# Kernel optimization log

Hardware: AMD Instinct MI355X
Metric: run time of the kernel (lower is better)

## Reference

```python
import jax, jax.numpy as jnp
import numpy as np

EPS = 1e-12  # matches torch.nn.functional.normalize default eps

B, SQ, SD, H, D = 64, 128, 1024, 768, 128


def setup_inputs() -> dict:
    key = jax.random.key(0)
    k1, k2, k3 = jax.random.split(key, 3)
    return {
        "query_hidden": jax.random.normal(k1, (B, SQ, H), dtype=jnp.float32),
        "query_attention_mask": jnp.ones((B, SQ), dtype=jnp.int32),
        "doc_hidden": jax.random.normal(k2, (B, SD, H), dtype=jnp.float32),
        "doc_attention_mask": jnp.ones((B, SD), dtype=jnp.int32),
        "W": jax.random.normal(k3, (D, H), dtype=jnp.float32) * (H ** -0.5),
    }


def _encode(hidden, mask, W):
    # mask padding tokens, project hidden_size -> colbert_dim, L2 normalize per token
    emb = hidden * mask[..., None].astype(hidden.dtype)          # [b, s, h]
    emb = jnp.einsum("bsh,dh->bsd", emb, W)                      # [b, s, d]
    norm = jnp.linalg.norm(emb, axis=-1, keepdims=True)
    return emb / jnp.maximum(norm, EPS)


def reference(query_hidden, query_attention_mask, doc_hidden, doc_attention_mask, W):
    q = _encode(query_hidden, query_attention_mask, W)           # [b, sq, d]
    dcc = _encode(doc_hidden, doc_attention_mask, W)             # [b, sd, d]
    sim = jnp.einsum("bsd,btd->bst", q, dcc)                     # [b, sq, sd]
    return sim.max(axis=2).sum(axis=1)                           # [b] MaxSim score
```

## Files before the change

kernel.cpp:

```cpp
#include <hip/hip_runtime.h>
#include <hip/hip_bf16.h>

#define NB 64
#define SQL 128
#define SDL 1024
#define HH 768
#define DD 128

typedef __attribute__((ext_vector_type(8))) short short8;
typedef __attribute__((ext_vector_type(4))) float f32x4;

__device__ __forceinline__ unsigned short bf16r(float f) {
    unsigned int u = __builtin_bit_cast(unsigned int, f);
    u += 0x7FFFu + ((u >> 16) & 1u);
    return (unsigned short)(u >> 16);
}

__global__ __launch_bounds__(256) void k_wconv(const float* __restrict__ W,
                                               unsigned short* __restrict__ Wb) {
    int i = blockIdx.x * 256 + threadIdx.x;
    float4 v = reinterpret_cast<const float4*>(W)[i];
    ushort4 o;
    o.x = bf16r(v.x); o.y = bf16r(v.y); o.z = bf16r(v.z); o.w = bf16r(v.w);
    reinterpret_cast<ushort4*>(Wb)[i] = o;
}

__global__ __launch_bounds__(256) void k_project(
        const float* __restrict__ qh, const int* __restrict__ qm,
        const float* __restrict__ dh, const int* __restrict__ dm,
        const unsigned short* __restrict__ Wb,
        unsigned short* __restrict__ qe, unsigned short* __restrict__ de) {
    int bx = blockIdx.x;
    int b = bx / 9;
    int seg = bx % 9;
    const float* src;
    const int* mask;
    unsigned short* dst;
    if (seg == 0) {
        src = qh + (size_t)b * SQL * HH;
        mask = qm + (size_t)b * SQL;
        dst = qe + (size_t)b * SQL * DD;
    } else {
        size_t off = (size_t)(seg - 1) * 128;
        src = dh + ((size_t)b * SDL + off) * HH;
        mask = dm + (size_t)b * SDL + off;
        dst = de + ((size_t)b * SDL + off) * DD;
    }

    int lane = threadIdx.x & 63;
    int w = threadIdx.x >> 6;
    int l15 = lane & 15;
    int lg = lane >> 4;

    f32x4 acc[8][2];
#pragma unroll
    for (int dt = 0; dt < 8; ++dt)
#pragma unroll
        for (int jt = 0; jt < 2; ++jt) acc[dt][jt] = (f32x4){0.f, 0.f, 0.f, 0.f};

    const float* rowp0 = src + (size_t)(w * 32 + l15) * HH;
    const float* rowp1 = src + (size_t)(w * 32 + 16 + l15) * HH;

    for (int ks = 0; ks < HH / 32; ++ks) {
        int k0 = ks * 32 + lg * 8;
        short8 hf[2];
        {
            float4 a0 = *reinterpret_cast<const float4*>(rowp0 + k0);
            float4 a1 = *reinterpret_cast<const float4*>(rowp0 + k0 + 4);
            short8 s;
            s[0] = (short)bf16r(a0.x); s[1] = (short)bf16r(a0.y);
            s[2] = (short)bf16r(a0.z); s[3] = (short)bf16r(a0.w);
            s[4] = (short)bf16r(a1.x); s[5] = (short)bf16r(a1.y);
            s[6] = (short)bf16r(a1.z); s[7] = (short)bf16r(a1.w);
            hf[0] = s;
        }
        {
            float4 a0 = *reinterpret_cast<const float4*>(rowp1 + k0);
            float4 a1 = *reinterpret_cast<const float4*>(rowp1 + k0 + 4);
            short8 s;
            s[0] = (short)bf16r(a0.x); s[1] = (short)bf16r(a0.y);
            s[2] = (short)bf16r(a0.z); s[3] = (short)bf16r(a0.w);
            s[4] = (short)bf16r(a1.x); s[5] = (short)bf16r(a1.y);
            s[6] = (short)bf16r(a1.z); s[7] = (short)bf16r(a1.w);
            hf[1] = s;
        }
#pragma unroll
        for (int dt = 0; dt < 8; ++dt) {
            short8 wf = *reinterpret_cast<const short8*>(Wb + (size_t)(dt * 16 + l15) * HH + k0);
            acc[dt][0] = __builtin_amdgcn_mfma_f32_16x16x32_bf16(wf, hf[0], acc[dt][0], 0, 0, 0);
            acc[dt][1] = __builtin_amdgcn_mfma_f32_16x16x32_bf16(wf, hf[1], acc[dt][1], 0, 0, 0);
        }
    }

#pragma unroll
    for (int jt = 0; jt < 2; ++jt) {
        float ss = 0.f;
#pragma unroll
        for (int dt = 0; dt < 8; ++dt) {
            ss += acc[dt][jt][0] * acc[dt][jt][0];
            ss += acc[dt][jt][1] * acc[dt][jt][1];
            ss += acc[dt][jt][2] * acc[dt][jt][2];
            ss += acc[dt][jt][3] * acc[dt][jt][3];
        }
        ss += __shfl_xor(ss, 16, 64);
        ss += __shfl_xor(ss, 32, 64);
        int tokl = w * 32 + jt * 16 + l15;
        int mk = mask[tokl];
        float scale = mk ? (1.0f / fmaxf(sqrtf(ss), 1e-12f)) : 0.0f;
        unsigned short* orow = dst + (size_t)tokl * DD + lg * 4;
#pragma unroll
        for (int dt = 0; dt < 8; ++dt) {
            ushort4 o;
            o.x = bf16r(acc[dt][jt][0] * scale);
            o.y = bf16r(acc[dt][jt][1] * scale);
            o.z = bf16r(acc[dt][jt][2] * scale);
            o.w = bf16r(acc[dt][jt][3] * scale);
            *reinterpret_cast<ushort4*>(orow + dt * 16) = o;
        }
    }
}

__global__ __launch_bounds__(256) void k_sim(const unsigned short* __restrict__ qe,
                                             const unsigned short* __restrict__ de,
                                             float* __restrict__ partial) {
    __shared__ uint4 qs[SQL * 16];
    __shared__ uint4 dsm[256 * 16];
    __shared__ float bm[4][SQL];

    int b = blockIdx.x >> 2;
    int c = blockIdx.x & 3;

    const uint4* qg = reinterpret_cast<const uint4*>(qe + (size_t)b * SQL * DD);
    for (int idx = threadIdx.x; idx < SQL * 16; idx += 256) {
        int row = idx >> 4, ch = idx & 15;
        qs[row * 16 + (ch ^ (row & 7))] = qg[idx];
    }
    const uint4* dg = reinterpret_cast<const uint4*>(de + ((size_t)b * SDL + (size_t)c * 256) * DD);
    for (int idx = threadIdx.x; idx < 256 * 16; idx += 256) {
        int row = idx >> 4, ch = idx & 15;
        dsm[row * 16 + (ch ^ (row & 7))] = dg[idx];
    }
    __syncthreads();

    int lane = threadIdx.x & 63;
    int w = threadIdx.x >> 6;
    int l15 = lane & 15;
    int lg = lane >> 4;

    float rmax[8][4];
#pragma unroll
    for (int i = 0; i < 8; ++i)
#pragma unroll
        for (int r = 0; r < 4; ++r) rmax[i][r] = -3.4e38f;

    for (int i = 0; i < 8; ++i) {
        short8 a[4];
        int arow = i * 16 + l15;
#pragma unroll
        for (int ks = 0; ks < 4; ++ks) {
            int ch = ks * 4 + lg;
            a[ks] = *reinterpret_cast<const short8*>(&qs[arow * 16 + (ch ^ (arow & 7))]);
        }
#pragma unroll
        for (int jj = 0; jj < 4; ++jj) {
            int drow = (w * 4 + jj) * 16 + l15;
            f32x4 accv = (f32x4){0.f, 0.f, 0.f, 0.f};
#pragma unroll
            for (int ks = 0; ks < 4; ++ks) {
                int ch = ks * 4 + lg;
                short8 bf = *reinterpret_cast<const short8*>(&dsm[drow * 16 + (ch ^ (drow & 7))]);
                accv = __builtin_amdgcn_mfma_f32_16x16x32_bf16(a[ks], bf, accv, 0, 0, 0);
            }
#pragma unroll
            for (int r = 0; r < 4; ++r) rmax[i][r] = fmaxf(rmax[i][r], accv[r]);
        }
    }

#pragma unroll
    for (int i = 0; i < 8; ++i) {
#pragma unroll
        for (int r = 0; r < 4; ++r) {
            float v = rmax[i][r];
            v = fmaxf(v, __shfl_xor(v, 1, 64));
            v = fmaxf(v, __shfl_xor(v, 2, 64));
            v = fmaxf(v, __shfl_xor(v, 4, 64));
            v = fmaxf(v, __shfl_xor(v, 8, 64));
            if (l15 == 0) bm[w][i * 16 + lg * 4 + r] = v;
        }
    }
    __syncthreads();

    if (threadIdx.x < SQL) {
        int sq = threadIdx.x;
        float m = fmaxf(fmaxf(bm[0][sq], bm[1][sq]), fmaxf(bm[2][sq], bm[3][sq]));
        partial[((size_t)b * 4 + c) * SQL + sq] = m;
    }
}

__global__ __launch_bounds__(128) void k_reduce(const float* __restrict__ partial,
                                                float* __restrict__ out) {
    int b = blockIdx.x;
    int sq = threadIdx.x;
    const float* p = partial + (size_t)b * 4 * SQL;
    float m = fmaxf(fmaxf(p[sq], p[SQL + sq]), fmaxf(p[2 * SQL + sq], p[3 * SQL + sq]));
    float s = m;
    s += __shfl_xor(s, 1, 64);
    s += __shfl_xor(s, 2, 64);
    s += __shfl_xor(s, 4, 64);
    s += __shfl_xor(s, 8, 64);
    s += __shfl_xor(s, 16, 64);
    s += __shfl_xor(s, 32, 64);
    __shared__ float tmp[2];
    int lane = threadIdx.x & 63;
    int wv = threadIdx.x >> 6;
    if (lane == 0) tmp[wv] = s;
    __syncthreads();
    if (threadIdx.x == 0) out[b] = tmp[0] + tmp[1];
}

extern "C" void kernel_launch(void* const* d_in, const int* in_sizes, int n_in,
                              void* d_out, int out_size, void* d_ws, size_t ws_size,
                              hipStream_t stream) {
    const float* qh = (const float*)d_in[0];
    const int* qm = (const int*)d_in[1];
    const float* dh = (const float*)d_in[2];
    const int* dm = (const int*)d_in[3];
    const float* W = (const float*)d_in[4];
    float* out = (float*)d_out;

    char* ws = (char*)d_ws;
    unsigned short* Wb = (unsigned short*)(ws);
    unsigned short* qe = (unsigned short*)(ws + 196608);
    unsigned short* de = (unsigned short*)(ws + 2293760);
    float* partial = (float*)(ws + 19070976);

    hipLaunchKernelGGL(k_wconv, dim3(96), dim3(256), 0, stream, W, Wb);
    hipLaunchKernelGGL(k_project, dim3(NB * 9), dim3(256), 0, stream,
                       qh, qm, dh, dm, Wb, qe, de);
    hipLaunchKernelGGL(k_sim, dim3(NB * 4), dim3(256), 0, stream, qe, de, partial);
    hipLaunchKernelGGL(k_reduce, dim3(NB), dim3(128), 0, stream, partial, out);
}
```

Baseline: 378.7 us.

## Split projection and sim blocks in half and software-pipeline hidden-state loads

The projection kernel now uses twice as many blocks, each covering 64 tokens with one 16-token tile per wave. The fp32 hidden-state loads are prefetched three k-steps ahead in registers so they overlap with the MFMAs, and launch bounds request 4 blocks per CU. The similarity kernel splits each batch into 8 doc chunks of 128 rows, halving shared memory per block and doubling the grid, and the reduce kernel now takes the max over 8 partials. The goal is more parallelism and hidden load latency on a memory-bound projection, at the cost of reloading W fragments per token tile and staging the query tile twice as often.

New measurement: 466.2 us. 23.1% more time.

```diff
diff --git a/kernel.cpp b/kernel.cpp
--- a/kernel.cpp
+++ b/kernel.cpp
@@ -14,6 +14,15 @@
     unsigned int u = __builtin_bit_cast(unsigned int, f);
     u += 0x7FFFu + ((u >> 16) & 1u);
     return (unsigned short)(u >> 16);
+}
+
+__device__ __forceinline__ short8 cvt8(float4 a, float4 b) {
+    short8 s;
+    s[0] = (short)bf16r(a.x); s[1] = (short)bf16r(a.y);
+    s[2] = (short)bf16r(a.z); s[3] = (short)bf16r(a.w);
+    s[4] = (short)bf16r(b.x); s[5] = (short)bf16r(b.y);
+    s[6] = (short)bf16r(b.z); s[7] = (short)bf16r(b.w);
+    return s;
 }
 
 __global__ __launch_bounds__(256) void k_wconv(const float* __restrict__ W,
@@ -25,14 +34,16 @@
     reinterpret_cast<ushort4*>(Wb)[i] = o;
 }
 
-__global__ __launch_bounds__(256) void k_project(
+__global__ __launch_bounds__(256, 4) void k_project(
         const float* __restrict__ qh, const int* __restrict__ qm,
         const float* __restrict__ dh, const int* __restrict__ dm,
         const unsigned short* __restrict__ Wb,
         unsigned short* __restrict__ qe, unsigned short* __restrict__ de) {
     int bx = blockIdx.x;
-    int b = bx / 9;
-    int seg = bx % 9;
+    int b = bx / 18;
+    int r = bx % 18;
+    int seg = r >> 1;
+    int half = r & 1;
     const float* src;
     const int* mask;
     unsigned short* dst;
@@ -51,72 +62,84 @@
     int w = threadIdx.x >> 6;
     int l15 = lane & 15;
     int lg = lane >> 4;
-
-    f32x4 acc[8][2];
-#pragma unroll
-    for (int dt = 0; dt < 8; ++dt)
-#pragma unroll
-        for (int jt = 0; jt < 2; ++jt) acc[dt][jt] = (f32x4){0.f, 0.f, 0.f, 0.f};
-
-    const float* rowp0 = src + (size_t)(w * 32 + l15) * HH;
-    const float* rowp1 = src + (size_t)(w * 32 + 16 + l15) * HH;
-
-    for (int ks = 0; ks < HH / 32; ++ks) {
-        int k0 = ks * 32 + lg * 8;
-        short8 hf[2];
+    int tok = half * 64 + w * 16 + l15;
+
+    const float* rp = src + (size_t)tok * HH + lg * 8;
+
+    f32x4 acc[8];
+#pragma unroll
+    for (int dt = 0; dt < 8; ++dt) acc[dt] = (f32x4){0.f, 0.f, 0.f, 0.f};
+
+    float4 pa0 = *reinterpret_cast<const float4*>(rp);
+    float4 pb0 = *reinterpret_cast<const float4*>(rp + 4);
+    float4 pa1 = *reinterpret_cast<const float4*>(rp + 32);
+    float4 pb1 = *reinterpret_cast<const float4*>(rp + 36);
+    float4 pa2 = *reinterpret_cast<const float4*>(rp + 64);
+    float4 pb2 = *reinterpret_cast<const float4*>(rp + 68);
+
+    for (int ks = 0; ks < 24; ks += 3) {
         {
-            float4 a0 = *reinterpret_cast<const float4*>(rowp0 + k0);
-            float4 a1 = *reinterpret_cast<const float4*>(rowp0 + k0 + 4);
-            short8 s;
-            s[0] = (short)bf16r(a0.x); s[1] = (short)bf16r(a0.y);
-            s[2] = (short)bf16r(a0.z); s[3] = (short)bf16r(a0.w);
-            s[4] = (short)bf16r(a1.x); s[5] = (short)bf16r(a1.y);
-            s[6] = (short)bf16r(a1.z); s[7] = (short)bf16r(a1.w);
-            hf[0] = s;
+            short8 h = cvt8(pa0, pb0);
+            int nk = ks + 3;
+            const float* np = rp + (size_t)(nk < 24 ? nk : 0) * 32;
+            pa0 = *reinterpret_cast<const float4*>(np);
+            pb0 = *reinterpret_cast<const float4*>(np + 4);
+            int k0 = ks * 32 + lg * 8;
+#pragma unroll
+            for (int dt = 0; dt < 8; ++dt) {
+                short8 wf = *reinterpret_cast<const short8*>(Wb + (size_t)(dt * 16 + l15) * HH + k0);
+                acc[dt] = __builtin_amdgcn_mfma_f32_16x16x32_bf16(wf, h, acc[dt], 0, 0, 0);
+            }
         }
         {
-            float4 a0 = *reinterpret_cast<const float4*>(rowp1 + k0);
-            float4 a1 = *reinterpret_cast<const float4*>(rowp1 + k0 + 4);
-            short8 s;
-            s[0] = (short)bf16r(a0.x); s[1] = (short)bf16r(a0.y);
-            s[2] = (short)bf16r(a0.z); s[3] = (short)bf16r(a0.w);
-            s[4] = (short)bf16r(a1.x); s[5] = (short)bf16r(a1.y);
-            s[6] = (short)bf16r(a1.z); s[7] = (short)bf16r(a1.w);
-            hf[1] = s;
-        }
-#pragma unroll
-        for (int dt = 0; dt < 8; ++dt) {
-            short8 wf = *reinterpret_cast<const short8*>(Wb + (size_t)(dt * 16 + l15) * HH + k0);
-            acc[dt][0] = __builtin_amdgcn_mfma_f32_16x16x32_bf16(wf, hf[0], acc[dt][0], 0, 0, 0);
-            acc[dt][1] = __builtin_amdgcn_mfma_f32_16x16x32_bf16(wf, hf[1], acc[dt][1], 0, 0, 0);
-        }
-    }
-
-#pragma unroll
-    for (int jt = 0; jt < 2; ++jt) {
-        float ss = 0.f;
-#pragma unroll
-        for (int dt = 0; dt < 8; ++dt) {
-            ss += acc[dt][jt][0] * acc[dt][jt][0];
-            ss += acc[dt][jt][1] * acc[dt][jt][1];
-            ss += acc[dt][jt][2] * acc[dt][jt][2];
-            ss += acc[dt][jt][3] * acc[dt][jt][3];
-        }
-        ss += __shfl_xor(ss, 16, 64);
-        ss += __shfl_xor(ss, 32, 64);
-        int tokl = w * 32 + jt * 16 + l15;
-        int mk = mask[tokl];
-        float scale = mk ? (1.0f / fmaxf(sqrtf(ss), 1e-12f)) : 0.0f;
-        unsigned short* orow = dst + (size_t)tokl * DD + lg * 4;
-#pragma unroll
-        for (int dt = 0; dt < 8; ++dt) {
-            ushort4 o;
-            o.x = bf16r(acc[dt][jt][0] * scale);
-            o.y = bf16r(acc[dt][jt][1] * scale);
-            o.z = bf16r(acc[dt][jt][2] * scale);
-            o.w = bf16r(acc[dt][jt][3] * scale);
-            *reinterpret_cast<ushort4*>(orow + dt * 16) = o;
-        }
+            short8 h = cvt8(pa1, pb1);
+            int nk = ks + 4;
+            const float* np = rp + (size_t)(nk < 24 ? nk : 0) * 32;
+            pa1 = *reinterpret_cast<const float4*>(np);
+            pb1 = *reinterpret_cast<const float4*>(np + 4);
+            int k0 = (ks + 1) * 32 + lg * 8;
+#pragma unroll
+            for (int dt = 0; dt < 8; ++dt) {
+                short8 wf = *reinterpret_cast<const short8*>(Wb + (size_t)(dt * 16 + l15) * HH + k0);
+                acc[dt] = __builtin_amdgcn_mfma_f32_16x16x32_bf16(wf, h, acc[dt], 0, 0, 0);
+            }
+        }
+        {
+            short8 h = cvt8(pa2, pb2);
+            int nk = ks + 5;
+            const float* np = rp + (size_t)(nk < 24 ? nk : 0) * 32;
+            pa2 = *reinterpret_cast<const float4*>(np);
+            pb2 = *reinterpret_cast<const float4*>(np + 4);
+            int k0 = (ks + 2) * 32 + lg * 8;
+#pragma unroll
+            for (int dt = 0; dt < 8; ++dt) {
+                short8 wf = *reinterpret_cast<const short8*>(Wb + (size_t)(dt * 16 + l15) * HH + k0);
+                acc[dt] = __builtin_amdgcn_mfma_f32_16x16x32_bf16(wf, h, acc[dt], 0, 0, 0);
+            }
+        }
+    }
+
+    float ss = 0.f;
+#pragma unroll
+    for (int dt = 0; dt < 8; ++dt) {
+        ss += acc[dt][0] * acc[dt][0];
+        ss += acc[dt][1] * acc[dt][1];
+        ss += acc[dt][2] * acc[dt][2];
+        ss += acc[dt][3] * acc[dt][3];
+    }
+    ss += __shfl_xor(ss, 16, 64);
+    ss += __shfl_xor(ss, 32, 64);
+    int mk = mask[tok];
+    float scale = mk ? (1.0f / fmaxf(sqrtf(ss), 1e-12f)) : 0.0f;
+    unsigned short* orow = dst + (size_t)tok * DD + lg * 4;
+#pragma unroll
+    for (int dt = 0; dt < 8; ++dt) {
+        ushort4 o;
+        o.x = bf16r(acc[dt][0] * scale);
+        o.y = bf16r(acc[dt][1] * scale);
+        o.z = bf16r(acc[dt][2] * scale);
+        o.w = bf16r(acc[dt][3] * scale);
+        *reinterpret_cast<ushort4*>(orow + dt * 16) = o;
     }
 }
 
@@ -124,19 +147,19 @@
                                              const unsigned short* __restrict__ de,
                                              float* __restrict__ partial) {
     __shared__ uint4 qs[SQL * 16];
-    __shared__ uint4 dsm[256 * 16];
+    __shared__ uint4 dsm[SQL * 16];
     __shared__ float bm[4][SQL];
 
-    int b = blockIdx.x >> 2;
-    int c = blockIdx.x & 3;
+    int b = blockIdx.x >> 3;
+    int c = blockIdx.x & 7;
 
     const uint4* qg = reinterpret_cast<const uint4*>(qe + (size_t)b * SQL * DD);
     for (int idx = threadIdx.x; idx < SQL * 16; idx += 256) {
         int row = idx >> 4, ch = idx & 15;
         qs[row * 16 + (ch ^ (row & 7))] = qg[idx];
     }
-    const uint4* dg = reinterpret_cast<const uint4*>(de + ((size_t)b * SDL + (size_t)c * 256) * DD);
-    for (int idx = threadIdx.x; idx < 256 * 16; idx += 256) {
+    const uint4* dg = reinterpret_cast<const uint4*>(de + ((size_t)b * SDL + (size_t)c * 128) * DD);
+    for (int idx = threadIdx.x; idx < SQL * 16; idx += 256) {
         int row = idx >> 4, ch = idx & 15;
         dsm[row * 16 + (ch ^ (row & 7))] = dg[idx];
     }
@@ -162,8 +185,8 @@
             a[ks] = *reinterpret_cast<const short8*>(&qs[arow * 16 + (ch ^ (arow & 7))]);
         }
 #pragma unroll
-        for (int jj = 0; jj < 4; ++jj) {
-            int drow = (w * 4 + jj) * 16 + l15;
+        for (int jj = 0; jj < 2; ++jj) {
+            int drow = (w * 2 + jj) * 16 + l15;
             f32x4 accv = (f32x4){0.f, 0.f, 0.f, 0.f};
 #pragma unroll
             for (int ks = 0; ks < 4; ++ks) {
@@ -193,7 +216,7 @@
     if (threadIdx.x < SQL) {
         int sq = threadIdx.x;
         float m = fmaxf(fmaxf(bm[0][sq], bm[1][sq]), fmaxf(bm[2][sq], bm[3][sq]));
-        partial[((size_t)b * 4 + c) * SQL + sq] = m;
+        partial[((size_t)b * 8 + c) * SQL + sq] = m;
     }
 }
 
@@ -201,8 +224,10 @@
                                                 float* __restrict__ out) {
     int b = blockIdx.x;
     int sq = threadIdx.x;
-    const float* p = partial + (size_t)b * 4 * SQL;
-    float m = fmaxf(fmaxf(p[sq], p[SQL + sq]), fmaxf(p[2 * SQL + sq], p[3 * SQL + sq]));
+    const float* p = partial + (size_t)b * 8 * SQL;
+    float m = -3.4e38f;
+#pragma unroll
+    for (int k = 0; k < 8; ++k) m = fmaxf(m, p[k * SQL + sq]);
     float s = m;
     s += __shfl_xor(s, 1, 64);
     s += __shfl_xor(s, 2, 64);
@@ -235,8 +260,8 @@
     float* partial = (float*)(ws + 19070976);
 
     hipLaunchKernelGGL(k_wconv, dim3(96), dim3(256), 0, stream, W, Wb);
-    hipLaunchKernelGGL(k_project, dim3(NB * 9), dim3(256), 0, stream,
+    hipLaunchKernelGGL(k_project, dim3(NB * 9 * 2), dim3(256), 0, stream,
                        qh, qm, dh, dm, Wb, qe, de);
-    hipLaunchKernelGGL(k_sim, dim3(NB * 4), dim3(256), 0, stream, qe, de, partial);
+    hipLaunchKernelGGL(k_sim, dim3(NB * 8), dim3(256), 0, stream, qe, de, partial);
     hipLaunchKernelGGL(k_reduce, dim3(NB), dim3(128), 0, stream, partial, out);
 }
```

## Stage W tiles through double-buffered LDS and prefetch activations in projection

Applied to the files above, without the earlier changes.

The projection kernel now copies bf16 W chunks of 64 K-columns into a double-buffered, XOR-swizzled LDS area instead of having every wave read W from global memory. It also software-prefetches the next activation float4 loads one step ahead, and adds an occupancy hint to launch bounds. Separately, the similarity kernel splits each batch into 8 doc chunks of 128 instead of 4 of 256, doubling the grid, and the reduce kernel folds 8 partials. The aim is less global/L2 traffic for W, better latency hiding and more blocks for the sim stage, at the cost of extra syncs per chunk and re-loading the query tile twice as often.

New measurement: 343.0 us. 1.1x faster.

```diff
diff --git a/kernel.cpp b/kernel.cpp
--- a/kernel.cpp
+++ b/kernel.cpp
@@ -14,6 +14,15 @@
     unsigned int u = __builtin_bit_cast(unsigned int, f);
     u += 0x7FFFu + ((u >> 16) & 1u);
     return (unsigned short)(u >> 16);
+}
+
+__device__ __forceinline__ short8 cvt8(float4 a, float4 b) {
+    short8 s;
+    s[0] = (short)bf16r(a.x); s[1] = (short)bf16r(a.y);
+    s[2] = (short)bf16r(a.z); s[3] = (short)bf16r(a.w);
+    s[4] = (short)bf16r(b.x); s[5] = (short)bf16r(b.y);
+    s[6] = (short)bf16r(b.z); s[7] = (short)bf16r(b.w);
+    return s;
 }
 
 __global__ __launch_bounds__(256) void k_wconv(const float* __restrict__ W,
@@ -25,11 +34,13 @@
     reinterpret_cast<ushort4*>(Wb)[i] = o;
 }
 
-__global__ __launch_bounds__(256) void k_project(
+__global__ __launch_bounds__(256, 3) void k_project(
         const float* __restrict__ qh, const int* __restrict__ qm,
         const float* __restrict__ dh, const int* __restrict__ dm,
         const unsigned short* __restrict__ Wb,
         unsigned short* __restrict__ qe, unsigned short* __restrict__ de) {
+    __shared__ unsigned short w_lds[2][8192];
+
     int bx = blockIdx.x;
     int b = bx / 9;
     int seg = bx % 9;
@@ -47,49 +58,108 @@
         dst = de + ((size_t)b * SDL + off) * DD;
     }
 
-    int lane = threadIdx.x & 63;
-    int w = threadIdx.x >> 6;
+    int tid = threadIdx.x;
+    int lane = tid & 63;
+    int w = tid >> 6;
     int l15 = lane & 15;
     int lg = lane >> 4;
 
+    int g0 = tid,        r0 = g0 >> 3, p0 = g0 & 7, s0i = p0 ^ (r0 & 7);
+    int g1 = tid + 256,  r1 = g1 >> 3, p1 = g1 & 7, s1i = p1 ^ (r1 & 7);
+    int g2 = tid + 512,  r2 = g2 >> 3, p2 = g2 & 7, s2i = p2 ^ (r2 & 7);
+    int g3 = tid + 768,  r3 = g3 >> 3, p3 = g3 & 7, s3i = p3 ^ (r3 & 7);
+    const unsigned short* wg0 = Wb + (size_t)r0 * HH + s0i * 8;
+    const unsigned short* wg1 = Wb + (size_t)r1 * HH + s1i * 8;
+    const unsigned short* wg2 = Wb + (size_t)r2 * HH + s2i * 8;
+    const unsigned short* wg3 = Wb + (size_t)r3 * HH + s3i * 8;
+    int lo0 = r0 * 64 + p0 * 8;
+    int lo1 = r1 * 64 + p1 * 8;
+    int lo2 = r2 * 64 + p2 * 8;
+    int lo3 = r3 * 64 + p3 * 8;
+
+    const float* rp0 = src + (size_t)(w * 32 + l15) * HH + lg * 8;
+    const float* rp1 = src + (size_t)(w * 32 + 16 + l15) * HH + lg * 8;
+
     f32x4 acc[8][2];
 #pragma unroll
-    for (int dt = 0; dt < 8; ++dt)
-#pragma unroll
-        for (int jt = 0; jt < 2; ++jt) acc[dt][jt] = (f32x4){0.f, 0.f, 0.f, 0.f};
-
-    const float* rowp0 = src + (size_t)(w * 32 + l15) * HH;
-    const float* rowp1 = src + (size_t)(w * 32 + 16 + l15) * HH;
-
-    for (int ks = 0; ks < HH / 32; ++ks) {
-        int k0 = ks * 32 + lg * 8;
-        short8 hf[2];
+    for (int dt = 0; dt < 8; ++dt) {
+        acc[dt][0] = (f32x4){0.f, 0.f, 0.f, 0.f};
+        acc[dt][1] = (f32x4){0.f, 0.f, 0.f, 0.f};
+    }
+
+    {
+        short8 t0 = *reinterpret_cast<const short8*>(wg0);
+        short8 t1 = *reinterpret_cast<const short8*>(wg1);
+        short8 t2 = *reinterpret_cast<const short8*>(wg2);
+        short8 t3 = *reinterpret_cast<const short8*>(wg3);
+        *reinterpret_cast<short8*>(&w_lds[0][lo0]) = t0;
+        *reinterpret_cast<short8*>(&w_lds[0][lo1]) = t1;
+        *reinterpret_cast<short8*>(&w_lds[0][lo2]) = t2;
+        *reinterpret_cast<short8*>(&w_lds[0][lo3]) = t3;
+    }
+    float4 pa0 = *reinterpret_cast<const float4*>(rp0);
+    float4 pb0 = *reinterpret_cast<const float4*>(rp0 + 4);
+    float4 pa1 = *reinterpret_cast<const float4*>(rp1);
+    float4 pb1 = *reinterpret_cast<const float4*>(rp1 + 4);
+    __syncthreads();
+
+    int buf = 0;
+    for (int c = 0; c < 12; ++c) {
+        short8 st0, st1, st2, st3;
+        if (c < 11) {
+            int ko = (c + 1) * 64;
+            st0 = *reinterpret_cast<const short8*>(wg0 + ko);
+            st1 = *reinterpret_cast<const short8*>(wg1 + ko);
+            st2 = *reinterpret_cast<const short8*>(wg2 + ko);
+            st3 = *reinterpret_cast<const short8*>(wg3 + ko);
+        }
         {
-            float4 a0 = *reinterpret_cast<const float4*>(rowp0 + k0);
-            float4 a1 = *reinterpret_cast<const float4*>(rowp0 + k0 + 4);
-            short8 s;
-            s[0] = (short)bf16r(a0.x); s[1] = (short)bf16r(a0.y);
-            s[2] = (short)bf16r(a0.z); s[3] = (short)bf16r(a0.w);
-            s[4] = (short)bf16r(a1.x); s[5] = (short)bf16r(a1.y);
-            s[6] = (short)bf16r(a1.z); s[7] = (short)bf16r(a1.w);
-            hf[0] = s;
+            short8 h0 = cvt8(pa0, pb0);
+            short8 h1 = cvt8(pa1, pb1);
+            int kk = c * 2;
+            const float* q0 = rp0 + (size_t)(kk + 1) * 32;
+            const float* q1 = rp1 + (size_t)(kk + 1) * 32;
+            pa0 = *reinterpret_cast<const float4*>(q0);
+            pb0 = *reinterpret_cast<const float4*>(q0 + 4);
+            pa1 = *reinterpret_cast<const float4*>(q1);
+            pb1 = *reinterpret_cast<const float4*>(q1 + 4);
+#pragma unroll
+            for (int dt = 0; dt < 8; ++dt) {
+                int row = dt * 16 + l15;
+                int gp = lg ^ (l15 & 7);
+                short8 wf = *reinterpret_cast<const short8*>(&w_lds[buf][row * 64 + gp * 8]);
+                acc[dt][0] = __builtin_amdgcn_mfma_f32_16x16x32_bf16(wf, h0, acc[dt][0], 0, 0, 0);
+                acc[dt][1] = __builtin_amdgcn_mfma_f32_16x16x32_bf16(wf, h1, acc[dt][1], 0, 0, 0);
+            }
         }
         {
-            float4 a0 = *reinterpret_cast<const float4*>(rowp1 + k0);
-            float4 a1 = *reinterpret_cast<const float4*>(rowp1 + k0 + 4);
-            short8 s;
-            s[0] = (short)bf16r(a0.x); s[1] = (short)bf16r(a0.y);
-            s[2] = (short)bf16r(a0.z); s[3] = (short)bf16r(a0.w);
-            s[4] = (short)bf16r(a1.x); s[5] = (short)bf16r(a1.y);
-            s[6] = (short)bf16r(a1.z); s[7] = (short)bf16r(a1.w);
-            hf[1] = s;
-        }
-#pragma unroll
-        for (int dt = 0; dt < 8; ++dt) {
-            short8 wf = *reinterpret_cast<const short8*>(Wb + (size_t)(dt * 16 + l15) * HH + k0);
-            acc[dt][0] = __builtin_amdgcn_mfma_f32_16x16x32_bf16(wf, hf[0], acc[dt][0], 0, 0, 0);
-            acc[dt][1] = __builtin_amdgcn_mfma_f32_16x16x32_bf16(wf, hf[1], acc[dt][1], 0, 0, 0);
-        }
+            short8 h0 = cvt8(pa0, pb0);
+            short8 h1 = cvt8(pa1, pb1);
+            int kk = c * 2 + 1;
+            int nk = (kk + 1 < 24) ? (kk + 1) : 0;
+            const float* q0 = rp0 + (size_t)nk * 32;
+            const float* q1 = rp1 + (size_t)nk * 32;
+            pa0 = *reinterpret_cast<const float4*>(q0);
+            pb0 = *reinterpret_cast<const float4*>(q0 + 4);
+            pa1 = *reinterpret_cast<const float4*>(q1);
+            pb1 = *reinterpret_cast<const float4*>(q1 + 4);
+#pragma unroll
+            for (int dt = 0; dt < 8; ++dt) {
+                int row = dt * 16 + l15;
+                int gp = (4 + lg) ^ (l15 & 7);
+                short8 wf = *reinterpret_cast<const short8*>(&w_lds[buf][row * 64 + gp * 8]);
+                acc[dt][0] = __builtin_amdgcn_mfma_f32_16x16x32_bf16(wf, h0, acc[dt][0], 0, 0, 0);
+                acc[dt][1] = __builtin_amdgcn_mfma_f32_16x16x32_bf16(wf, h1, acc[dt][1], 0, 0, 0);
+            }
+        }
+        if (c < 11) {
+            *reinterpret_cast<short8*>(&w_lds[buf ^ 1][lo0]) = st0;
+            *reinterpret_cast<short8*>(&w_lds[buf ^ 1][lo1]) = st1;
+            *reinterpret_cast<short8*>(&w_lds[buf ^ 1][lo2]) = st2;
+            *reinterpret_cast<short8*>(&w_lds[buf ^ 1][lo3]) = st3;
+        }
+        __syncthreads();
+        buf ^= 1;
     }
 
 #pragma unroll
@@ -124,19 +194,19 @@
                                              const unsigned short* __restrict__ de,
                                              float* __restrict__ partial) {
     __shared__ uint4 qs[SQL * 16];
-    __shared__ uint4 dsm[256 * 16];
+    __shared__ uint4 dsm[SQL * 16];
     __shared__ float bm[4][SQL];
 
-    int b = blockIdx.x >> 2;
-    int c = blockIdx.x & 3;
+    int b = blockIdx.x >> 3;
+    int c = blockIdx.x & 7;
 
     const uint4* qg = reinterpret_cast<const uint4*>(qe + (size_t)b * SQL * DD);
     for (int idx = threadIdx.x; idx < SQL * 16; idx += 256) {
         int row = idx >> 4, ch = idx & 15;
         qs[row * 16 + (ch ^ (row & 7))] = qg[idx];
     }
-    const uint4* dg = reinterpret_cast<const uint4*>(de + ((size_t)b * SDL + (size_t)c * 256) * DD);
-    for (int idx = threadIdx.x; idx < 256 * 16; idx += 256) {
+    const uint4* dg = reinterpret_cast<const uint4*>(de + ((size_t)b * SDL + (size_t)c * 128) * DD);
+    for (int idx = threadIdx.x; idx < SQL * 16; idx += 256) {
         int row = idx >> 4, ch = idx & 15;
         dsm[row * 16 + (ch ^ (row & 7))] = dg[idx];
     }
@@ -162,8 +232,8 @@
             a[ks] = *reinterpret_cast<const short8*>(&qs[arow * 16 + (ch ^ (arow & 7))]);
         }
 #pragma unroll
-        for (int jj = 0; jj < 4; ++jj) {
-            int drow = (w * 4 + jj) * 16 + l15;
+        for (int jj = 0; jj < 2; ++jj) {
+            int drow = (w * 2 + jj) * 16 + l15;
             f32x4 accv = (f32x4){0.f, 0.f, 0.f, 0.f};
 #pragma unroll
             for (int ks = 0; ks < 4; ++ks) {
@@ -193,7 +263,7 @@
     if (threadIdx.x < SQL) {
         int sq = threadIdx.x;
         float m = fmaxf(fmaxf(bm[0][sq], bm[1][sq]), fmaxf(bm[2][sq], bm[3][sq]));
-        partial[((size_t)b * 4 + c) * SQL + sq] = m;
+        partial[((size_t)b * 8 + c) * SQL + sq] = m;
     }
 }
 
@@ -201,8 +271,10 @@
                                                 float* __restrict__ out) {
     int b = blockIdx.x;
     int sq = threadIdx.x;
-    const float* p = partial + (size_t)b * 4 * SQL;
-    float m = fmaxf(fmaxf(p[sq], p[SQL + sq]), fmaxf(p[2 * SQL + sq], p[3 * SQL + sq]));
+    const float* p = partial + (size_t)b * 8 * SQL;
+    float m = -3.4e38f;
+#pragma unroll
+    for (int k = 0; k < 8; ++k) m = fmaxf(m, p[k * SQL + sq]);
     float s = m;
     s += __shfl_xor(s, 1, 64);
     s += __shfl_xor(s, 2, 64);
@@ -237,6 +309,6 @@
     hipLaunchKernelGGL(k_wconv, dim3(96), dim3(256), 0, stream, W, Wb);
     hipLaunchKernelGGL(k_project, dim3(NB * 9), dim3(256), 0, stream,
                        qh, qm, dh, dm, Wb, qe, de);
-    hipLaunchKernelGGL(k_sim, dim3(NB * 4), dim3(256), 0, stream, qe, de, partial);
+    hipLaunchKernelGGL(k_sim, dim3(NB * 8), dim3(256), 0, stream, qe, de, partial);
     hipLaunchKernelGGL(k_reduce, dim3(NB), dim3(128), 0, stream, partial, out);
 }
```

## Stage W tiles in double-buffered LDS with prefetched activations; split sim grid finer

Applied to the files above, without the earlier changes.

The projection kernel now stages 128-wide K chunks of the bf16 weight matrix into a swizzled, double-buffered shared-memory tile. It prefetches the fp32 activation rows four K-steps ahead in registers so global loads overlap the MFMA work, replacing the per-lane global reads of W. The similarity kernel is split into 8 doc chunks per batch instead of 4, doubling the grid to 512 blocks, and the reduce kernel is updated to combine 8 partials. This trades more LDS use and register pressure (launch bounds asking for 2 blocks per CU) and a barrier per chunk for better memory-latency hiding and occupancy.

After: 334.9 us. 1.13x faster.

```diff
diff --git a/kernel.cpp b/kernel.cpp
--- a/kernel.cpp
+++ b/kernel.cpp
@@ -14,6 +14,15 @@
     unsigned int u = __builtin_bit_cast(unsigned int, f);
     u += 0x7FFFu + ((u >> 16) & 1u);
     return (unsigned short)(u >> 16);
+}
+
+__device__ __forceinline__ short8 cvt8(float4 a, float4 b) {
+    short8 s;
+    s[0] = (short)bf16r(a.x); s[1] = (short)bf16r(a.y);
+    s[2] = (short)bf16r(a.z); s[3] = (short)bf16r(a.w);
+    s[4] = (short)bf16r(b.x); s[5] = (short)bf16r(b.y);
+    s[6] = (short)bf16r(b.z); s[7] = (short)bf16r(b.w);
+    return s;
 }
 
 __global__ __launch_bounds__(256) void k_wconv(const float* __restrict__ W,
@@ -25,11 +34,13 @@
     reinterpret_cast<ushort4*>(Wb)[i] = o;
 }
 
-__global__ __launch_bounds__(256) void k_project(
+__global__ __launch_bounds__(256, 2) void k_project(
         const float* __restrict__ qh, const int* __restrict__ qm,
         const float* __restrict__ dh, const int* __restrict__ dm,
         const unsigned short* __restrict__ Wb,
         unsigned short* __restrict__ qe, unsigned short* __restrict__ de) {
+    __shared__ unsigned short w_lds[2][16384];
+
     int bx = blockIdx.x;
     int b = bx / 9;
     int seg = bx % 9;
@@ -47,50 +58,94 @@
         dst = de + ((size_t)b * SDL + off) * DD;
     }
 
-    int lane = threadIdx.x & 63;
-    int w = threadIdx.x >> 6;
+    int tid = threadIdx.x;
+    int lane = tid & 63;
+    int w = tid >> 6;
     int l15 = lane & 15;
     int lg = lane >> 4;
 
+    int row0 = tid >> 4;
+    int pos  = tid & 15;
+    int sg   = pos ^ row0;
+    const unsigned short* wsrc = Wb + (size_t)row0 * HH + sg * 8;
+    int ldsoff = row0 * 128 + pos * 8;
+
+    const float* rp0 = src + (size_t)(w * 32 + l15) * HH + lg * 8;
+    const float* rp1 = src + (size_t)(w * 32 + 16 + l15) * HH + lg * 8;
+
     f32x4 acc[8][2];
 #pragma unroll
-    for (int dt = 0; dt < 8; ++dt)
-#pragma unroll
-        for (int jt = 0; jt < 2; ++jt) acc[dt][jt] = (f32x4){0.f, 0.f, 0.f, 0.f};
-
-    const float* rowp0 = src + (size_t)(w * 32 + l15) * HH;
-    const float* rowp1 = src + (size_t)(w * 32 + 16 + l15) * HH;
-
-    for (int ks = 0; ks < HH / 32; ++ks) {
-        int k0 = ks * 32 + lg * 8;
-        short8 hf[2];
-        {
-            float4 a0 = *reinterpret_cast<const float4*>(rowp0 + k0);
-            float4 a1 = *reinterpret_cast<const float4*>(rowp0 + k0 + 4);
-            short8 s;
-            s[0] = (short)bf16r(a0.x); s[1] = (short)bf16r(a0.y);
-            s[2] = (short)bf16r(a0.z); s[3] = (short)bf16r(a0.w);
-            s[4] = (short)bf16r(a1.x); s[5] = (short)bf16r(a1.y);
-            s[6] = (short)bf16r(a1.z); s[7] = (short)bf16r(a1.w);
-            hf[0] = s;
-        }
-        {
-            float4 a0 = *reinterpret_cast<const float4*>(rowp1 + k0);
-            float4 a1 = *reinterpret_cast<const float4*>(rowp1 + k0 + 4);
-            short8 s;
-            s[0] = (short)bf16r(a0.x); s[1] = (short)bf16r(a0.y);
-            s[2] = (short)bf16r(a0.z); s[3] = (short)bf16r(a0.w);
-            s[4] = (short)bf16r(a1.x); s[5] = (short)bf16r(a1.y);
-            s[6] = (short)bf16r(a1.z); s[7] = (short)bf16r(a1.w);
-            hf[1] = s;
-        }
-#pragma unroll
-        for (int dt = 0; dt < 8; ++dt) {
-            short8 wf = *reinterpret_cast<const short8*>(Wb + (size_t)(dt * 16 + l15) * HH + k0);
-            acc[dt][0] = __builtin_amdgcn_mfma_f32_16x16x32_bf16(wf, hf[0], acc[dt][0], 0, 0, 0);
-            acc[dt][1] = __builtin_amdgcn_mfma_f32_16x16x32_bf16(wf, hf[1], acc[dt][1], 0, 0, 0);
-        }
-    }
+    for (int dt = 0; dt < 8; ++dt) {
+        acc[dt][0] = (f32x4){0.f, 0.f, 0.f, 0.f};
+        acc[dt][1] = (f32x4){0.f, 0.f, 0.f, 0.f};
+    }
+
+#pragma unroll
+    for (int j = 0; j < 8; ++j) {
+        short8 t = *reinterpret_cast<const short8*>(wsrc + (size_t)j * 16 * HH);
+        *reinterpret_cast<short8*>(&w_lds[0][ldsoff + j * 2048]) = t;
+    }
+    float4 a0A = *reinterpret_cast<const float4*>(rp0);
+    float4 b0A = *reinterpret_cast<const float4*>(rp0 + 4);
+    float4 a1A = *reinterpret_cast<const float4*>(rp1);
+    float4 b1A = *reinterpret_cast<const float4*>(rp1 + 4);
+    float4 a0B = *reinterpret_cast<const float4*>(rp0 + 32);
+    float4 b0B = *reinterpret_cast<const float4*>(rp0 + 36);
+    float4 a1B = *reinterpret_cast<const float4*>(rp1 + 32);
+    float4 b1B = *reinterpret_cast<const float4*>(rp1 + 36);
+    float4 a0C = *reinterpret_cast<const float4*>(rp0 + 64);
+    float4 b0C = *reinterpret_cast<const float4*>(rp0 + 68);
+    float4 a1C = *reinterpret_cast<const float4*>(rp1 + 64);
+    float4 b1C = *reinterpret_cast<const float4*>(rp1 + 68);
+    float4 a0D = *reinterpret_cast<const float4*>(rp0 + 96);
+    float4 b0D = *reinterpret_cast<const float4*>(rp0 + 100);
+    float4 a1D = *reinterpret_cast<const float4*>(rp1 + 96);
+    float4 b1D = *reinterpret_cast<const float4*>(rp1 + 100);
+    __syncthreads();
+
+#define KSTEP(A0_, B0_, A1_, B1_, KSIDX, NEXTKK)                               \
+    {                                                                          \
+        short8 h0 = cvt8(A0_, B0_);                                            \
+        short8 h1 = cvt8(A1_, B1_);                                            \
+        int nk = (NEXTKK) < 24 ? (NEXTKK) : 0;                                 \
+        const float* q0 = rp0 + (size_t)nk * 32;                               \
+        const float* q1 = rp1 + (size_t)nk * 32;                               \
+        A0_ = *reinterpret_cast<const float4*>(q0);                            \
+        B0_ = *reinterpret_cast<const float4*>(q0 + 4);                        \
+        A1_ = *reinterpret_cast<const float4*>(q1);                            \
+        B1_ = *reinterpret_cast<const float4*>(q1 + 4);                        \
+        _Pragma("unroll")                                                      \
+        for (int dt = 0; dt < 8; ++dt) {                                       \
+            int p = ((KSIDX) * 4 + lg) ^ l15;                                  \
+            short8 wf = *reinterpret_cast<const short8*>(                      \
+                &w_lds[buf][(dt * 16 + l15) * 128 + p * 8]);                   \
+            acc[dt][0] = __builtin_amdgcn_mfma_f32_16x16x32_bf16(wf, h0, acc[dt][0], 0, 0, 0); \
+            acc[dt][1] = __builtin_amdgcn_mfma_f32_16x16x32_bf16(wf, h1, acc[dt][1], 0, 0, 0); \
+        }                                                                      \
+    }
+
+    int buf = 0;
+    for (int c = 0; c < 6; ++c) {
+        short8 st[8];
+        if (c < 5) {
+            int ko = (c + 1) * 128;
+#pragma unroll
+            for (int j = 0; j < 8; ++j)
+                st[j] = *reinterpret_cast<const short8*>(wsrc + (size_t)j * 16 * HH + ko);
+        }
+        KSTEP(a0A, b0A, a1A, b1A, 0, 4 * c + 4)
+        KSTEP(a0B, b0B, a1B, b1B, 1, 4 * c + 5)
+        KSTEP(a0C, b0C, a1C, b1C, 2, 4 * c + 6)
+        KSTEP(a0D, b0D, a1D, b1D, 3, 4 * c + 7)
+        if (c < 5) {
+#pragma unroll
+            for (int j = 0; j < 8; ++j)
+                *reinterpret_cast<short8*>(&w_lds[buf ^ 1][ldsoff + j * 2048]) = st[j];
+        }
+        __syncthreads();
+        buf ^= 1;
+    }
+#undef KSTEP
 
 #pragma unroll
     for (int jt = 0; jt < 2; ++jt) {
@@ -124,19 +179,19 @@
                                              const unsigned short* __restrict__ de,
                                              float* __restrict__ partial) {
     __shared__ uint4 qs[SQL * 16];
-    __shared__ uint4 dsm[256 * 16];
+    __shared__ uint4 dsm[SQL * 16];
     __shared__ float bm[4][SQL];
 
-    int b = blockIdx.x >> 2;
-    int c = blockIdx.x & 3;
+    int b = blockIdx.x >> 3;
+    int c = blockIdx.x & 7;
 
     const uint4* qg = reinterpret_cast<const uint4*>(qe + (size_t)b * SQL * DD);
     for (int idx = threadIdx.x; idx < SQL * 16; idx += 256) {
         int row = idx >> 4, ch = idx & 15;
         qs[row * 16 + (ch ^ (row & 7))] = qg[idx];
     }
-    const uint4* dg = reinterpret_cast<const uint4*>(de + ((size_t)b * SDL + (size_t)c * 256) * DD);
-    for (int idx = threadIdx.x; idx < 256 * 16; idx += 256) {
+    const uint4* dg = reinterpret_cast<const uint4*>(de + ((size_t)b * SDL + (size_t)c * 128) * DD);
+    for (int idx = threadIdx.x; idx < SQL * 16; idx += 256) {
         int row = idx >> 4, ch = idx & 15;
         dsm[row * 16 + (ch ^ (row & 7))] = dg[idx];
     }
@@ -162,8 +217,8 @@
             a[ks] = *reinterpret_cast<const short8*>(&qs[arow * 16 + (ch ^ (arow & 7))]);
         }
 #pragma unroll
-        for (int jj = 0; jj < 4; ++jj) {
-            int drow = (w * 4 + jj) * 16 + l15;
+        for (int jj = 0; jj < 2; ++jj) {
+            int drow = (w * 2 + jj) * 16 + l15;
             f32x4 accv = (f32x4){0.f, 0.f, 0.f, 0.f};
 #pragma unroll
             for (int ks = 0; ks < 4; ++ks) {
@@ -193,7 +248,7 @@
     if (threadIdx.x < SQL) {
         int sq = threadIdx.x;
         float m = fmaxf(fmaxf(bm[0][sq], bm[1][sq]), fmaxf(bm[2][sq], bm[3][sq]));
-        partial[((size_t)b * 4 + c) * SQL + sq] = m;
+        partial[((size_t)b * 8 + c) * SQL + sq] = m;
     }
 }
 
@@ -201,8 +256,10 @@
                                                 float* __restrict__ out) {
     int b = blockIdx.x;
     int sq = threadIdx.x;
-    const float* p = partial + (size_t)b * 4 * SQL;
-    float m = fmaxf(fmaxf(p[sq], p[SQL + sq]), fmaxf(p[2 * SQL + sq], p[3 * SQL + sq]));
+    const float* p = partial + (size_t)b * 8 * SQL;
+    float m = -3.4e38f;
+#pragma unroll
+    for (int k = 0; k < 8; ++k) m = fmaxf(m, p[k * SQL + sq]);
     float s = m;
     s += __shfl_xor(s, 1, 64);
     s += __shfl_xor(s, 2, 64);
@@ -237,6 +294,6 @@
     hipLaunchKernelGGL(k_wconv, dim3(96), dim3(256), 0, stream, W, Wb);
     hipLaunchKernelGGL(k_project, dim3(NB * 9), dim3(256), 0, stream,
                        qh, qm, dh, dm, Wb, qe, de);
-    hipLaunchKernelGGL(k_sim, dim3(NB * 4), dim3(256), 0, stream, qe, de, partial);
+    hipLaunchKernelGGL(k_sim, dim3(NB * 8), dim3(256), 0, stream, qe, de, partial);
     hipLaunchKernelGGL(k_reduce, dim3(NB), dim3(128), 0, stream, partial, out);
 }
```
